# Kernel tuning notes

Measured on AMD Instinct MI355X. Metric: run time of the kernel, lower is better.

Reference implementation:

```python
import jax, jax.numpy as jnp
import numpy as np

B, N, H = 64, 1024, 64
ALPHA = 0.2  # leaky relu negative slope
NEG_BIG = -1.0e12


def setup_inputs() -> dict:
    key = jax.random.key(0)
    k1, k2, k3, k4, k5, k6 = jax.random.split(key, 6)
    inp = jax.random.normal(k1, (B, N, H), dtype=jnp.float32)
    inp_none = jax.random.normal(k2, (B, N, H), dtype=jnp.float32)
    A = (jax.random.uniform(k3, (B, N, N)) < 0.1).astype(jnp.float32)
    # per-sample [i, j] ranges, i <= j < N
    l = jnp.sort(jax.random.randint(k4, (B, 2), 0, N), axis=1)
    # xavier_uniform with gain=1.414 on shape (2H, 1)
    bound = 1.414 * np.sqrt(6.0 / (2 * H + 1))
    a_i = jax.random.uniform(k5, (2 * H, 1), minval=-bound, maxval=bound, dtype=jnp.float32)
    a_c = jax.random.uniform(k6, (2 * H, 1), minval=-bound, maxval=bound, dtype=jnp.float32)
    return {"inp": inp, "inp_none": inp_none, "A": A, "l": l, "a_i": a_i, "a_c": a_c}


def reference(inp, inp_none, A, l, a_i, a_c):
    h = inp.shape[-1]
    n = inp.shape[1]
    # additive-score halves: [B, N, 1]
    Wh1_i = inp_none @ a_i[:h]
    Wh2_i = inp @ a_i[h:]
    Wh1_c = inp @ a_c[:h]
    Wh2_c = inp @ a_c[h:]
    # vectorized replacement of the per-sample range overwrite loop:
    # rows in [l[b,0], l[b,1]) take the a_i branch
    pos = jnp.arange(n)[None, :, None]                       # [1, N, 1]
    in_range = (pos >= l[:, 0, None, None]) & (pos < l[:, 1, None, None])  # [B, N, 1]
    Wh1 = jnp.where(in_range, Wh1_i, Wh1_c)                  # [B, N, 1]
    Wh2 = jnp.where(in_range, Wh2_i, Wh2_c)                  # [B, N, 1]
    # e[b, p, q] = leakyrelu((Wh1[b,p] + Wh2[b,q]) * A[b,p,q])
    e = (Wh1 + jnp.swapaxes(Wh2, 1, 2)) * A                  # [B, N, N]
    e = jnp.where(e >= 0, e, ALPHA * e)
    attn = jnp.where(A > 0, e, NEG_BIG)
    attn = jax.nn.softmax(attn, axis=2)
    h_prime = attn @ inp                                     # [B, N, H]
    return jax.nn.elu(h_prime)  # concat=True
```

## Files before the change

### kernel.cpp

```cpp
#include <hip/hip_runtime.h>
#include <hip/hip_bf16.h>
#include <math.h>
#include <stdint.h>

constexpr int Bn = 64, Nn = 1024, Hn = 64;
constexpr float LRELU_ALPHA = 0.2f;

typedef __attribute__((ext_vector_type(8))) short bf16x8;
typedef __attribute__((ext_vector_type(4))) float f32x4;

__device__ __forceinline__ float lrelu(float x) { return x >= 0.f ? x : LRELU_ALPHA * x; }
__device__ __forceinline__ ushort f2bf(float x) {
    uint u = __float_as_uint(x);
    return (ushort)((u + 0x7FFFu + ((u >> 16) & 1u)) >> 16);
}
__device__ __forceinline__ float bf2f(ushort b) { return __uint_as_float(((uint)b) << 16); }

#define LDS_BARRIER()                                             \
    do {                                                          \
        asm volatile("s_waitcnt lgkmcnt(0)" ::: "memory");        \
        __builtin_amdgcn_s_barrier();                             \
        asm volatile("" ::: "memory");                            \
    } while (0)

__global__ __launch_bounds__(256) void prep_kernel(
    const float* __restrict__ inp, const float* __restrict__ inp_none,
    const int* __restrict__ l, const float* __restrict__ a_i,
    const float* __restrict__ a_c,
    ushort* __restrict__ inpT, float* __restrict__ Wh1, float* __restrict__ Wh2)
{
    __shared__ ushort tile[64][74];
    const int b  = blockIdx.x >> 4;
    const int q0 = (blockIdx.x & 15) << 6;
    const int t  = threadIdx.x;
    const int l0 = l[b * 2], l1 = l[b * 2 + 1];

    {
        const int q    = t >> 2;
        const int h0   = (t & 3) << 4;
        const int grow = q0 + q;
        const bool in_range = (grow >= l0) && (grow < l1);

        const float* src  = inp + ((size_t)(b * Nn + grow) * Hn + h0);
        const float* av2p = (in_range ? a_i : a_c) + Hn + h0;
        uint* dst = (uint*)&tile[q][h0];

        float p1 = 0.f, p2 = 0.f;
        #pragma unroll
        for (int i = 0; i < 4; ++i) {
            const float4 v = *(const float4*)(src + 4 * i);
            dst[2 * i + 0] = (uint)f2bf(v.x) | ((uint)f2bf(v.y) << 16);
            dst[2 * i + 1] = (uint)f2bf(v.z) | ((uint)f2bf(v.w) << 16);
            const float4 a2 = *(const float4*)(av2p + 4 * i);
            p2 += (v.x * a2.x + v.y * a2.y) + (v.z * a2.z + v.w * a2.w);
        }
        if (in_range) {
            const float* s1 = inp_none + ((size_t)(b * Nn + grow) * Hn + h0);
            #pragma unroll
            for (int i = 0; i < 4; ++i) {
                const float4 v1 = *(const float4*)(s1 + 4 * i);
                const float4 a1 = *(const float4*)(a_i + h0 + 4 * i);
                p1 += (v1.x * a1.x + v1.y * a1.y) + (v1.z * a1.z + v1.w * a1.w);
            }
        } else {
            const float* s1 = inp + ((size_t)(b * Nn + grow) * Hn + h0);
            #pragma unroll
            for (int i = 0; i < 4; ++i) {
                const float4 v1 = *(const float4*)(s1 + 4 * i);
                const float4 a1 = *(const float4*)(a_c + h0 + 4 * i);
                p1 += (v1.x * a1.x + v1.y * a1.y) + (v1.z * a1.z + v1.w * a1.w);
            }
        }
        p1 += __shfl_xor(p1, 1); p1 += __shfl_xor(p1, 2);
        p2 += __shfl_xor(p2, 1); p2 += __shfl_xor(p2, 2);
        if ((t & 3) == 0) {
            Wh1[b * Nn + grow] = p1;
            Wh2[b * Nn + grow] = p2;
        }
    }
    __syncthreads();
    {
        const int h  = t >> 2;
        const int qb = (t & 3) << 4;
        uint w[8];
        #pragma unroll
        for (int i = 0; i < 8; ++i)
            w[i] = (uint)tile[qb + 2 * i][h] | ((uint)tile[qb + 2 * i + 1][h] << 16);
        uint4* dst = (uint4*)(inpT + ((size_t)(b * Hn + h) * Nn + q0 + qb));
        dst[0] = make_uint4(w[0], w[1], w[2], w[3]);
        dst[1] = make_uint4(w[4], w[5], w[6], w[7]);
    }
}

__global__ __launch_bounds__(256, 6) void gat_mfma_kernel(
    const float* __restrict__ A, const ushort* __restrict__ inpT,
    const float* __restrict__ Wh1, const float* __restrict__ Wh2,
    float* __restrict__ out)
{
    __shared__ __align__(16) char pool[21632];
    float* wh2_lds = (float*)(pool + 16384);
    float* rs_part = (float*)(pool + 20480);
    float* inv_lds = (float*)(pool + 21504);
    float* out_lds = (float*)pool;

    const int t    = threadIdx.x;
    const int wave = t >> 6;
    const int lane = t & 63;

    const int d = blockIdx.x;
    const int o = (d & 7) * 256 + (d >> 3);
    const int b  = o >> 5;
    const int p0 = (o & 31) << 5;

    const float*  Ab   = A + (size_t)b * Nn * Nn;
    const float*  Wh2b = Wh2 + b * Nn;
    const ushort* Tb   = inpT + (size_t)b * Hn * Nn;

    const int r  = t >> 3;
    const int qo = (t & 7) << 2;
    const float wh1_r = Wh1[b * Nn + p0 + r];
    const float* Arow = Ab + (size_t)(p0 + r) * Nn;

    const int l15 = lane & 15;
    const int lg  = lane >> 4;
    const ushort* a_src = Tb + (size_t)(wave * 16 + l15) * Nn + lg * 8;
    const uint bswz = ((uint)(l15 & 7)) << 4;
    const uint row0 = (uint)(l15 * 512);
    const uint row1 = (uint)((l15 + 16) * 512);

    float4 aReg[8];
    #pragma unroll
    for (int j = 0; j < 8; ++j) aReg[j] = *(const float4*)(Arow + qo + 32 * j);
    #pragma unroll
    for (int w = 0; w < 4; ++w) wh2_lds[w * 256 + t] = Wh2b[w * 256 + t];
    LDS_BARRIER();

    f32x4 acc0 = {0.f, 0.f, 0.f, 0.f};
    f32x4 acc1 = {0.f, 0.f, 0.f, 0.f};
    float rs_local = 0.f;

    #pragma unroll
    for (int c = 0; c < 4; ++c) {
        #pragma unroll
        for (int j = 0; j < 8; ++j) {
            const int qq = qo + 32 * j;
            const float4 a4 = aReg[j];
            const float4 w2 = *(const float4*)(wh2_lds + c * 256 + qq);
            const float s0 = lrelu(wh1_r + w2.x);
            const float s1 = lrelu(wh1_r + w2.y);
            const float s2 = lrelu(wh1_r + w2.z);
            const float s3 = lrelu(wh1_r + w2.w);
            const ushort u0 = f2bf(a4.x > 0.f ? __expf(s0) : 0.f);
            const ushort u1 = f2bf(a4.y > 0.f ? __expf(s1) : 0.f);
            const ushort u2 = f2bf(a4.z > 0.f ? __expf(s2) : 0.f);
            const ushort u3 = f2bf(a4.w > 0.f ? __expf(s3) : 0.f);
            rs_local += (bf2f(u0) + bf2f(u1)) + (bf2f(u2) + bf2f(u3));
            const uint lo = (uint)u0 | ((uint)u1 << 16);
            const uint hi = (uint)u2 | ((uint)u3 << 16);
            const uint byte = ((uint)(r * 512 + qq * 2)) ^ (((uint)(r & 7)) << 4);
            *(uint2*)(pool + byte) = make_uint2(lo, hi);
        }
        if (c < 3) {
            #pragma unroll
            for (int j = 0; j < 8; ++j)
                aReg[j] = *(const float4*)(Arow + (c + 1) * 256 + qo + 32 * j);
        }
        LDS_BARRIER();

        #pragma unroll
        for (int kk = 0; kk < 8; ++kk) {
            const uint col = ((uint)(lg * 16 + kk * 64)) ^ bswz;
            const bf16x8 af = *(const bf16x8*)(a_src + c * 256 + kk * 32);
            const bf16x8 b0 = *(const bf16x8*)(pool + (row0 + col));
            const bf16x8 b1 = *(const bf16x8*)(pool + (row1 + col));
            acc0 = __builtin_amdgcn_mfma_f32_16x16x32_bf16(af, b0, acc0, 0, 0, 0);
            acc1 = __builtin_amdgcn_mfma_f32_16x16x32_bf16(af, b1, acc1, 0, 0, 0);
        }
        LDS_BARRIER();
    }

    rs_part[t] = rs_local;
    __syncthreads();
    if (t < 32) {
        float s = 0.f;
        #pragma unroll
        for (int j = 0; j < 8; ++j) s += rs_part[t * 8 + j];
        inv_lds[t] = s > 0.f ? 1.f / s : 0.f;
    }
    __syncthreads();

    #pragma unroll
    for (int nt = 0; nt < 2; ++nt) {
        const int p = nt * 16 + l15;
        const float inv = inv_lds[p];
        const f32x4 a = nt ? acc1 : acc0;
        #pragma unroll
        for (int rg = 0; rg < 4; ++rg) {
            const int h = wave * 16 + lg * 4 + rg;
            out_lds[p * 65 + h] = a[rg] * inv;
        }
    }
    __syncthreads();

    {
        const int p  = t >> 3;
        const int h0 = (t & 7) << 3;
        float v[8];
        #pragma unroll
        for (int i = 0; i < 8; ++i) {
            const float x = out_lds[p * 65 + h0 + i];
            v[i] = x > 0.f ? x : expm1f(x);
        }
        float* orow = out + (size_t)(b * Nn + p0 + p) * Hn + h0;
        *(float4*)(orow)     = make_float4(v[0], v[1], v[2], v[3]);
        *(float4*)(orow + 4) = make_float4(v[4], v[5], v[6], v[7]);
    }
}

__global__ __launch_bounds__(256) void wh_kernel(
    const float* __restrict__ inp, const float* __restrict__ inp_none,
    const int* __restrict__ l, const float* __restrict__ a_i,
    const float* __restrict__ a_c,
    float* __restrict__ Wh1, float* __restrict__ Wh2)
{
    const int wave = threadIdx.x >> 6;
    const int lane = threadIdx.x & 63;
    const int row  = blockIdx.x * 4 + wave;
    const int b    = row >> 10;
    const int n    = row & (Nn - 1);
    const int l0 = l[b * 2], l1 = l[b * 2 + 1];
    const bool in_range = (n >= l0) && (n < l1);
    const size_t base = (size_t)row * Hn + lane;
    const float x1  = in_range ? inp_none[base] : inp[base];
    const float x2  = inp[base];
    const float av1 = in_range ? a_i[lane]      : a_c[lane];
    const float av2 = in_range ? a_i[Hn + lane] : a_c[Hn + lane];
    float p1 = x1 * av1;
    float p2 = x2 * av2;
    #pragma unroll
    for (int off = 32; off > 0; off >>= 1) {
        p1 += __shfl_xor(p1, off);
        p2 += __shfl_xor(p2, off);
    }
    if (lane == 0) { Wh1[row] = p1; Wh2[row] = p2; }
}

__global__ __launch_bounds__(256) void gat_fallback_kernel(
    const float* __restrict__ inp, const float* __restrict__ A,
    const float* __restrict__ Wh1, const float* __restrict__ Wh2,
    float* __restrict__ out)
{
    __shared__ float wlds[4][256];
    __shared__ int   qlds[4][256];
    const int wave = threadIdx.x >> 6;
    const int lane = threadIdx.x & 63;
    const int cpx = gridDim.x >> 3;
    const int bid = blockIdx.x;
    const int swz = (bid & 7) * cpx + (bid >> 3);
    const int row = swz * 4 + wave;
    const int b   = row >> 10;
    const int p   = row & (Nn - 1);
    const float* Arow = A + ((size_t)b * Nn + p) * Nn;
    const float* Wh2b = Wh2 + b * Nn;
    const float  wh1p = Wh1[b * Nn + p];
    float4 sv[4];
    float  m = -INFINITY;
    #pragma unroll
    for (int k = 0; k < 4; ++k) {
        const int q0 = k * 256 + lane * 4;
        const float4 a4 = *(const float4*)(Arow + q0);
        const float4 w2 = *(const float4*)(Wh2b + q0);
        float4 s;
        s.x = (a4.x > 0.f) ? lrelu(wh1p + w2.x) : -INFINITY;
        s.y = (a4.y > 0.f) ? lrelu(wh1p + w2.y) : -INFINITY;
        s.z = (a4.z > 0.f) ? lrelu(wh1p + w2.z) : -INFINITY;
        s.w = (a4.w > 0.f) ? lrelu(wh1p + w2.w) : -INFINITY;
        sv[k] = s;
        m = fmaxf(m, fmaxf(fmaxf(s.x, s.y), fmaxf(s.z, s.w)));
    }
    #pragma unroll
    for (int off = 32; off > 0; off >>= 1) m = fmaxf(m, __shfl_xor(m, off));
    const bool empty = (m == -INFINITY);
    const float* inpb = inp + (size_t)b * Nn * Hn;
    float acc0 = 0.f, acc1 = 0.f;
    if (!empty) {
        float4 wv[4];
        float  lsum = 0.f;
        #pragma unroll
        for (int k = 0; k < 4; ++k) {
            float4 s = sv[k];
            float4 w;
            w.x = __expf(s.x - m); w.y = __expf(s.y - m);
            w.z = __expf(s.z - m); w.w = __expf(s.w - m);
            wv[k] = w;
            lsum += (w.x + w.y) + (w.z + w.w);
        }
        #pragma unroll
        for (int off = 32; off > 0; off >>= 1) lsum += __shfl_xor(lsum, off);
        const float inv = 1.f / lsum;
        int c = 0;
        #pragma unroll
        for (int k = 0; k < 4; ++k)
            #pragma unroll
            for (int cc = 0; cc < 4; ++cc)
                c += (((const float*)&wv[k])[cc] != 0.f) ? 1 : 0;
        int s = c;
        #pragma unroll
        for (int off = 1; off < 64; off <<= 1) {
            const int tt = __shfl_up(s, off);
            if (lane >= off) s += tt;
        }
        int j   = s - c;
        int cnt = __shfl(s, 63);
        #pragma unroll
        for (int k = 0; k < 4; ++k)
            #pragma unroll
            for (int cc = 0; cc < 4; ++cc) {
                const float w = ((const float*)&wv[k])[cc];
                if (w != 0.f && j < 256) {
                    wlds[wave][j] = w;
                    qlds[wave][j] = (k * 256 + lane * 4 + cc) * Hn;
                    ++j;
                }
            }
        if (cnt > 256) cnt = 256;
        asm volatile("s_waitcnt lgkmcnt(0)" ::: "memory");
        int i = 0;
        for (; i + 4 <= cnt; i += 4) {
            const float w0 = wlds[wave][i], w1 = wlds[wave][i + 1];
            const float w2 = wlds[wave][i + 2], w3 = wlds[wave][i + 3];
            const int o0 = qlds[wave][i], o1 = qlds[wave][i + 1];
            const int o2 = qlds[wave][i + 2], o3 = qlds[wave][i + 3];
            acc0 = fmaf(w0, inpb[o0 + lane], acc0);
            acc1 = fmaf(w1, inpb[o1 + lane], acc1);
            acc0 = fmaf(w2, inpb[o2 + lane], acc0);
            acc1 = fmaf(w3, inpb[o3 + lane], acc1);
        }
        for (; i < cnt; ++i)
            acc0 = fmaf(wlds[wave][i], inpb[qlds[wave][i] + lane], acc0);
        acc0 = (acc0 + acc1) * inv;
    } else {
        for (int q = 0; q < Nn; ++q) acc0 += inpb[q * Hn + lane];
        acc0 *= (1.f / Nn);
    }
    const float rr = acc0 > 0.f ? acc0 : expm1f(acc0);
    out[(size_t)row * Hn + lane] = rr;
}

extern "C" void kernel_launch(void* const* d_in, const int* in_sizes, int n_in,
                              void* d_out, int out_size, void* d_ws, size_t ws_size,
                              hipStream_t stream) {
    const float* inp      = (const float*)d_in[0];
    const float* inp_none = (const float*)d_in[1];
    const float* A        = (const float*)d_in[2];
    const int*   l        = (const int*)d_in[3];
    const float* a_i      = (const float*)d_in[4];
    const float* a_c      = (const float*)d_in[5];
    float* out = (float*)d_out;

    float*  Wh1  = (float*)d_ws;
    float*  Wh2  = Wh1 + Bn * Nn;
    ushort* inpT = (ushort*)((char*)d_ws + (size_t)2 * Bn * Nn * 4);

    const size_t need = (size_t)2 * Bn * Nn * 4 + (size_t)Bn * Hn * Nn * 2;

    if (ws_size >= need) {
        prep_kernel<<<Bn * 16, 256, 0, stream>>>(inp, inp_none, l, a_i, a_c,
                                                 inpT, Wh1, Wh2);
        gat_mfma_kernel<<<Bn * 32, 256, 0, stream>>>(A, inpT, Wh1, Wh2, out);
    } else {
        wh_kernel<<<Bn * Nn / 4, 256, 0, stream>>>(inp, inp_none, l, a_i, a_c, Wh1, Wh2);
        gat_fallback_kernel<<<Bn * Nn / 4, 256, 0, stream>>>(inp, A, Wh1, Wh2, out);
    }
}
```

Baseline: 417.7 us.

## Precompute a bitmask of the adjacency matrix to shrink main-kernel loads

Adds a streaming pre-pass that reads the fp32 adjacency matrix once and packs its nonzero pattern into a 1-bit-per-entry mask. The attention kernel then loads 32x less mask data per row block instead of 32 float4 registers of A. This is meant to cut register pressure and memory latency inside the MFMA kernel. Launch bounds drop from 6 to 4 waves per SIMD, and LDS is compacted by reusing the Wh2 region for the reduction scratch. The cost is an extra kernel launch and an extra bitmask write and read on top of the full pass over A.

```diff
diff --git a/kernel.cpp b/kernel.cpp
--- a/kernel.cpp
+++ b/kernel.cpp
@@ -22,6 +22,27 @@
         __builtin_amdgcn_s_barrier();                             \
         asm volatile("" ::: "memory");                            \
     } while (0)
+
+__global__ __launch_bounds__(256) void amask_kernel(const float* __restrict__ A,
+                                                    uint* __restrict__ bm)
+{
+    const size_t g = (size_t)blockIdx.x * 256 + threadIdx.x;
+    const int lane = threadIdx.x & 63;
+    const float4 v0 = *(const float4*)(A + g * 8);
+    const float4 v1 = *(const float4*)(A + g * 8 + 4);
+    uint b = 0;
+    b |= (v0.x > 0.f) ? 1u   : 0u;
+    b |= (v0.y > 0.f) ? 2u   : 0u;
+    b |= (v0.z > 0.f) ? 4u   : 0u;
+    b |= (v0.w > 0.f) ? 8u   : 0u;
+    b |= (v1.x > 0.f) ? 16u  : 0u;
+    b |= (v1.y > 0.f) ? 32u  : 0u;
+    b |= (v1.z > 0.f) ? 64u  : 0u;
+    b |= (v1.w > 0.f) ? 128u : 0u;
+    uint t = b | (__shfl_xor(b, 1) << 8);
+    uint u = t | (__shfl_xor(t, 2) << 16);
+    if ((lane & 3) == 0) bm[g >> 2] = u;
+}
 
 __global__ __launch_bounds__(256) void prep_kernel(
     const float* __restrict__ inp, const float* __restrict__ inp_none,
@@ -92,15 +113,20 @@
     }
 }
 
-__global__ __launch_bounds__(256, 6) void gat_mfma_kernel(
-    const float* __restrict__ A, const ushort* __restrict__ inpT,
+__device__ __forceinline__ uint jw(const uint4& W0, const uint4& W1, int j) {
+    return (j == 0) ? W0.x : (j == 1) ? W0.y : (j == 2) ? W0.z : (j == 3) ? W0.w
+         : (j == 4) ? W1.x : (j == 5) ? W1.y : (j == 6) ? W1.z : W1.w;
+}
+
+__global__ __launch_bounds__(256, 4) void gat_mfma_kernel(
+    const uint* __restrict__ bm, const ushort* __restrict__ inpT,
     const float* __restrict__ Wh1, const float* __restrict__ Wh2,
     float* __restrict__ out)
 {
-    __shared__ __align__(16) char pool[21632];
+    __shared__ __align__(16) char pool[20480];
     float* wh2_lds = (float*)(pool + 16384);
-    float* rs_part = (float*)(pool + 20480);
-    float* inv_lds = (float*)(pool + 21504);
+    float* rs_part = (float*)(pool + 16384);
+    float* inv_lds = (float*)(pool + 16384 + 1024);
     float* out_lds = (float*)pool;
 
     const int t    = threadIdx.x;
@@ -112,14 +138,13 @@
     const int b  = o >> 5;
     const int p0 = (o & 31) << 5;
 
-    const float*  Ab   = A + (size_t)b * Nn * Nn;
     const float*  Wh2b = Wh2 + b * Nn;
     const ushort* Tb   = inpT + (size_t)b * Hn * Nn;
 
-    const int r  = t >> 3;
-    const int qo = (t & 7) << 2;
+    const int r = t >> 3;
+    const int u = t & 7;
     const float wh1_r = Wh1[b * Nn + p0 + r];
-    const float* Arow = Ab + (size_t)(p0 + r) * Nn;
+    const uint* bmrow = bm + (size_t)(b * Nn + p0 + r) * 32;
 
     const int l15 = lane & 15;
     const int lg  = lane >> 4;
@@ -128,9 +153,8 @@
     const uint row0 = (uint)(l15 * 512);
     const uint row1 = (uint)((l15 + 16) * 512);
 
-    float4 aReg[8];
-    #pragma unroll
-    for (int j = 0; j < 8; ++j) aReg[j] = *(const float4*)(Arow + qo + 32 * j);
+    uint4 W0 = *(const uint4*)(bmrow);
+    uint4 W1 = *(const uint4*)(bmrow + 4);
     #pragma unroll
     for (int w = 0; w < 4; ++w) wh2_lds[w * 256 + t] = Wh2b[w * 256 + t];
     LDS_BARRIER();
@@ -143,17 +167,17 @@
     for (int c = 0; c < 4; ++c) {
         #pragma unroll
         for (int j = 0; j < 8; ++j) {
-            const int qq = qo + 32 * j;
-            const float4 a4 = aReg[j];
+            const uint nib = (jw(W0, W1, j) >> (u * 4)) & 15u;
+            const int  qq  = u * 4 + 32 * j;
             const float4 w2 = *(const float4*)(wh2_lds + c * 256 + qq);
-            const float s0 = lrelu(wh1_r + w2.x);
-            const float s1 = lrelu(wh1_r + w2.y);
-            const float s2 = lrelu(wh1_r + w2.z);
-            const float s3 = lrelu(wh1_r + w2.w);
-            const ushort u0 = f2bf(a4.x > 0.f ? __expf(s0) : 0.f);
-            const ushort u1 = f2bf(a4.y > 0.f ? __expf(s1) : 0.f);
-            const ushort u2 = f2bf(a4.z > 0.f ? __expf(s2) : 0.f);
-            const ushort u3 = f2bf(a4.w > 0.f ? __expf(s3) : 0.f);
+            const float e0 = __expf(lrelu(wh1_r + w2.x));
+            const float e1 = __expf(lrelu(wh1_r + w2.y));
+            const float e2 = __expf(lrelu(wh1_r + w2.z));
+            const float e3 = __expf(lrelu(wh1_r + w2.w));
+            const ushort u0 = (nib & 1u) ? f2bf(e0) : (ushort)0;
+            const ushort u1 = (nib & 2u) ? f2bf(e1) : (ushort)0;
+            const ushort u2 = (nib & 4u) ? f2bf(e2) : (ushort)0;
+            const ushort u3 = (nib & 8u) ? f2bf(e3) : (ushort)0;
             rs_local += (bf2f(u0) + bf2f(u1)) + (bf2f(u2) + bf2f(u3));
             const uint lo = (uint)u0 | ((uint)u1 << 16);
             const uint hi = (uint)u2 | ((uint)u3 << 16);
@@ -161,9 +185,8 @@
             *(uint2*)(pool + byte) = make_uint2(lo, hi);
         }
         if (c < 3) {
-            #pragma unroll
-            for (int j = 0; j < 8; ++j)
-                aReg[j] = *(const float4*)(Arow + (c + 1) * 256 + qo + 32 * j);
+            W0 = *(const uint4*)(bmrow + (c + 1) * 8);
+            W1 = *(const uint4*)(bmrow + (c + 1) * 8 + 4);
         }
         LDS_BARRIER();
 
@@ -358,16 +381,20 @@
     const float* a_c      = (const float*)d_in[5];
     float* out = (float*)d_out;
 
-    float*  Wh1  = (float*)d_ws;
-    float*  Wh2  = Wh1 + Bn * Nn;
-    ushort* inpT = (ushort*)((char*)d_ws + (size_t)2 * Bn * Nn * 4);
-
-    const size_t need = (size_t)2 * Bn * Nn * 4 + (size_t)Bn * Hn * Nn * 2;
+    char* ws = (char*)d_ws;
+    float*  Wh1  = (float*)ws;
+    float*  Wh2  = (float*)(ws + (size_t)Bn * Nn * 4);
+    ushort* inpT = (ushort*)(ws + (size_t)2 * Bn * Nn * 4);
+    uint*   bmp  = (uint*)(ws + (size_t)2 * Bn * Nn * 4 + (size_t)Bn * Hn * Nn * 2);
+
+    const size_t need = (size_t)2 * Bn * Nn * 4 + (size_t)Bn * Hn * Nn * 2
+                      + (size_t)Bn * Nn * (Nn / 8);
 
     if (ws_size >= need) {
+        amask_kernel<<<Bn * Nn * Nn / 8 / 256, 256, 0, stream>>>(A, bmp);
         prep_kernel<<<Bn * 16, 256, 0, stream>>>(inp, inp_none, l, a_i, a_c,
                                                  inpT, Wh1, Wh2);
-        gat_mfma_kernel<<<Bn * 32, 256, 0, stream>>>(A, inpT, Wh1, Wh2, out);
+        gat_mfma_kernel<<<Bn * 32, 256, 0, stream>>>(bmp, inpT, Wh1, Wh2, out);
     } else {
         wh_kernel<<<Bn * Nn / 4, 256, 0, stream>>>(inp, inp_none, l, a_i, a_c, Wh1, Wh2);
         gat_fallback_kernel<<<Bn * Nn / 4, 256, 0, stream>>>(inp, A, Wh1, Wh2, out);
```

Result: no change. 421.9 us (+1.0%).
